# Optimization experiments

Measured on AMD Instinct MI355X. Metric: run time of the kernel, lower is better.

Reference implementation:

```python
import jax, jax.numpy as jnp
import numpy as np

N_NODES = 50000
N_EDGES = 800000
IN_SIZE = 128
HIDDEN = 128   # out_size * 2
OUT_SIZE = 64


def setup_inputs() -> dict:
    key = jax.random.key(0)
    ks = jax.random.split(key, 6)
    h = jax.random.normal(ks[0], (N_NODES, IN_SIZE), dtype=jnp.float32)
    W1 = jax.random.normal(ks[1], (IN_SIZE, HIDDEN), dtype=jnp.float32) * (1.0 / np.sqrt(IN_SIZE))
    b1 = jnp.zeros((HIDDEN,), dtype=jnp.float32)
    W2 = jax.random.normal(ks[2], (HIDDEN, OUT_SIZE), dtype=jnp.float32) * (1.0 / np.sqrt(HIDDEN))
    b2 = jnp.zeros((OUT_SIZE,), dtype=jnp.float32)
    src = jax.random.randint(ks[3], (N_EDGES,), 0, N_NODES, dtype=jnp.int64)
    dst = jax.random.randint(ks[4], (N_EDGES,), 0, N_NODES, dtype=jnp.int64)
    return {"h": h, "W1": W1, "b1": b1, "W2": W2, "b2": b2, "src": src, "dst": dst}


def _norms(src, dst, n_nodes):
    # DGL GraphConv norm='both': scale by out_degree^{-1/2} (src side)
    # and in_degree^{-1/2} (dst side); zero degrees clamped to 1.
    ones = jnp.ones(src.shape, dtype=jnp.float32)
    out_deg = jnp.maximum(jax.ops.segment_sum(ones, src, num_segments=n_nodes), 1.0)
    in_deg = jnp.maximum(jax.ops.segment_sum(ones, dst, num_segments=n_nodes), 1.0)
    return (out_deg ** -0.5)[:, None], (in_deg ** -0.5)[:, None]


def _graph_conv(x, W, b, src, dst, norm_out, norm_in, n_nodes):
    # h' = D_in^{-1/2} A D_out^{-1/2} x W + b
    x = x * norm_out                                   # [N, F]
    agg = jax.ops.segment_sum(x[src], dst, num_segments=n_nodes)  # SpMM: [N, F]
    return (agg * norm_in) @ W + b


def reference(h, W1, b1, W2, b2, src, dst):
    n_nodes = h.shape[0]
    norm_out, norm_in = _norms(src, dst, n_nodes)
    h = jax.nn.relu(_graph_conv(h, W1, b1, src, dst, norm_out, norm_in, n_nodes))
    h = jax.nn.relu(_graph_conv(h, W2, b2, src, dst, norm_out, norm_in, n_nodes))
    return h
```

## Files before the change

### kernel.cpp

```cpp
#include <hip/hip_runtime.h>

#define N_NODES 50000
#define N_EDGES 800000
#define CHUNKS 128
#define CHUNK_EDGES 6250
#define NBS 196
#define GA_BLOCKS 391
#define PLACE_BLOCKS 3125

typedef __attribute__((ext_vector_type(8))) short bf16x8;
typedef __attribute__((ext_vector_type(4))) float f32x4;

static __device__ inline unsigned short bf16_rne(float x) {
    unsigned ua = __float_as_uint(x);
    return (unsigned short)((ua + 0x7fffu + ((ua >> 16) & 1u)) >> 16);
}

static __device__ inline unsigned short f16_bits(float x) {
    _Float16 hx = (_Float16)x;
    return __builtin_bit_cast(unsigned short, hx);
}

static __device__ inline float2 unpack_f16x2(unsigned u) {
    _Float16 lo = __builtin_bit_cast(_Float16, (unsigned short)(u & 0xffffu));
    _Float16 hi = __builtin_bit_cast(_Float16, (unsigned short)(u >> 16));
    return make_float2((float)lo, (float)hi);
}

__global__ __launch_bounds__(1024) void hist_wpack_kernel(const int* __restrict__ src,
                                                          const int* __restrict__ dst,
                                                          unsigned char* __restrict__ cntD,
                                                          unsigned char* __restrict__ cntS,
                                                          unsigned char* __restrict__ rp,
                                                          const float* __restrict__ W1,
                                                          const float* __restrict__ W2,
                                                          unsigned short* __restrict__ wf_hi,
                                                          unsigned short* __restrict__ wf_lo,
                                                          unsigned short* __restrict__ wf2_hi,
                                                          unsigned short* __restrict__ wf2_lo) {
    const int t = threadIdx.x;
    const int c = blockIdx.x;

    if (c >= CHUNKS) {
        int idx = (c - CHUNKS) * 1024 + t;
        if (idx < 2048) {
            int l  = idx & 63;
            int ct = (idx >> 6) & 7;
            int ks = idx >> 9;
            int col = ct * 16 + (l & 15);
            int k0  = ks * 32 + (l >> 4) * 8;
            unsigned short hi[8], lo[8];
            #pragma unroll
            for (int j = 0; j < 8; ++j) {
                float x = W1[(size_t)(k0 + j) * 128 + col];
                unsigned short h16 = bf16_rne(x);
                hi[j] = h16;
                lo[j] = bf16_rne(x - __uint_as_float((unsigned)h16 << 16));
            }
            ((uint4*)wf_hi)[idx] = *(const uint4*)hi;
            ((uint4*)wf_lo)[idx] = *(const uint4*)lo;
        } else if (idx < 3072) {
            int i2 = idx - 2048;
            int l  = i2 & 63;
            int ct = (i2 >> 6) & 3;
            int ks = i2 >> 8;
            int col = ct * 16 + (l & 15);
            int k0  = ks * 32 + (l >> 4) * 8;
            unsigned short hi[8], lo[8];
            #pragma unroll
            for (int j = 0; j < 8; ++j) {
                float x = W2[(size_t)(k0 + j) * 64 + col];
                unsigned short h16 = bf16_rne(x);
                hi[j] = h16;
                lo[j] = bf16_rne(x - __uint_as_float((unsigned)h16 << 16));
            }
            ((uint4*)wf2_hi)[i2] = *(const uint4*)hi;
            ((uint4*)wf2_lo)[i2] = *(const uint4*)lo;
        }
        return;
    }

    __shared__ unsigned hD[12500];
    __shared__ unsigned hS[12500];
    for (int i = t; i < 12500; i += 1024) { hD[i] = 0u; hS[i] = 0u; }
    __syncthreads();

    const int base = c * CHUNK_EDGES;
    for (int i = t; i < CHUNK_EDGES; i += 1024) {
        int e = base + i;
        int d = dst[e];
        int s = src[e];
        unsigned shd = (unsigned)(d & 3) * 8u;
        unsigned old = atomicAdd(&hD[d >> 2], 1u << shd);
        rp[e] = (unsigned char)((old >> shd) & 0xffu);
        atomicAdd(&hS[s >> 2], 1u << ((unsigned)(s & 3) * 8u));
    }
    __syncthreads();

    unsigned* gD = (unsigned*)cntD + (size_t)c * 12500;
    unsigned* gS = (unsigned*)cntS + (size_t)c * 12500;
    for (int i = t; i < 12500; i += 1024) { gD[i] = hD[i]; gS[i] = hS[i]; }
}

__global__ __launch_bounds__(256) void deg_scan_kernel(unsigned char* __restrict__ cntD,
                                                       const unsigned char* __restrict__ cntS,
                                                       int* __restrict__ row_ptr,
                                                       int* __restrict__ bsum,
                                                       float* __restrict__ norm_out,
                                                       float* __restrict__ norm_in) {
    const int t = threadIdx.x, lane = t & 63, w = t >> 6;
    const int n = blockIdx.x * 256 + t;
    unsigned sumD = 0u, sumS = 0u;
    if (n < N_NODES) {
        #pragma unroll 4
        for (int c = 0; c < CHUNKS; ++c) {
            size_t idx = (size_t)c * 50000 + n;
            unsigned v = cntD[idx];
            cntD[idx] = (unsigned char)sumD;
            sumD += v;
            sumS += cntS[idx];
        }
        norm_in[n]  = rsqrtf((float)(sumD ? sumD : 1u));
        norm_out[n] = rsqrtf((float)(sumS ? sumS : 1u));
    }
    __shared__ int wsum[4];
    int v = (n < N_NODES) ? (int)sumD : 0;
    int incl = v;
    #pragma unroll
    for (int d = 1; d < 64; d <<= 1) {
        int u = __shfl_up(incl, d, 64);
        if (lane >= d) incl += u;
    }
    if (lane == 63) wsum[w] = incl;
    __syncthreads();
    int woff = 0, total = 0;
    #pragma unroll
    for (int j = 0; j < 4; ++j) {
        int s = wsum[j];
        if (j < w) woff += s;
        total += s;
    }
    if (n < N_NODES) row_ptr[n] = woff + incl - v;
    if (t == 0) bsum[blockIdx.x] = total;
}

__global__ __launch_bounds__(64) void scan2_kernel(int* __restrict__ bsum,
                                                   int* __restrict__ row_ptr) {
    const int lane = threadIdx.x;
    int carry = 0;
    for (int base = 0; base < NBS; base += 64) {
        int t = base + lane;
        int v = (t < NBS) ? bsum[t] : 0;
        int incl = v;
        #pragma unroll
        for (int d = 1; d < 64; d <<= 1) {
            int u = __shfl_up(incl, d, 64);
            if (lane >= d) incl += u;
        }
        int excl = carry + incl - v;
        if (t < NBS) bsum[t] = excl;
        if (t == NBS - 1) row_ptr[N_NODES] = N_EDGES - excl;
        carry += __shfl(incl, 63, 64);
    }
}

__global__ __launch_bounds__(256) void gemmA_place_kernel(const float* __restrict__ h,
                                                          const unsigned short* __restrict__ wf_hi,
                                                          const unsigned short* __restrict__ wf_lo,
                                                          const float* __restrict__ norm_out,
                                                          unsigned short* __restrict__ t1,
                                                          const int* __restrict__ src,
                                                          const int* __restrict__ dst,
                                                          const int* __restrict__ row_ptr,
                                                          const int* __restrict__ bsum,
                                                          const unsigned char* __restrict__ cntD,
                                                          const unsigned char* __restrict__ rp,
                                                          int* __restrict__ eidx) {
    if (blockIdx.x >= GA_BLOCKS) {
        int e = (blockIdx.x - GA_BLOCKS) * 256 + threadIdx.x;
        if (e < N_EDGES) {
            int d = dst[e];
            int c = e / CHUNK_EDGES;
            int pos = row_ptr[d] + bsum[d >> 8] + (int)cntD[(size_t)c * 50000 + d]
                    + (int)rp[e];
            eidx[pos] = src[e];
        }
        return;
    }

    const int t  = threadIdx.x;
    const int wv = t >> 6;
    const int l  = t & 63;
    const int lrow = l & 15;
    const int g    = l >> 4;
    const int n0 = blockIdx.x * 128 + wv * 32;

    int r0 = n0 + lrow;      if (r0 > N_NODES - 1) r0 = N_NODES - 1;
    int r1 = n0 + 16 + lrow; if (r1 > N_NODES - 1) r1 = N_NODES - 1;
    const float* h0 = h + (size_t)r0 * 128 + g * 8;
    const float* h1 = h + (size_t)r1 * 128 + g * 8;

    f32x4 acc[2][8];
    #pragma unroll
    for (int rt = 0; rt < 2; ++rt)
        #pragma unroll
        for (int ct = 0; ct < 8; ++ct)
            acc[rt][ct] = (f32x4){0.f, 0.f, 0.f, 0.f};

    const bf16x8* bh_base = (const bf16x8*)wf_hi;
    const bf16x8* bl_base = (const bf16x8*)wf_lo;

    for (int ks = 0; ks < 4; ++ks) {
        float a0[8], a1[8];
        *(float4*)(a0)     = *(const float4*)(h0 + ks * 32);
        *(float4*)(a0 + 4) = *(const float4*)(h0 + ks * 32 + 4);
        *(float4*)(a1)     = *(const float4*)(h1 + ks * 32);
        *(float4*)(a1 + 4) = *(const float4*)(h1 + ks * 32 + 4);

        bf16x8 a0h, a0l, a1h, a1l;
        #pragma unroll
        for (int j = 0; j < 8; ++j) {
            unsigned short hh = bf16_rne(a0[j]);
            a0h[j] = (short)hh;
            a0l[j] = (short)bf16_rne(a0[j] - __uint_as_float((unsigned)hh << 16));
            unsigned short h2 = bf16_rne(a1[j]);
            a1h[j] = (short)h2;
            a1l[j] = (short)bf16_rne(a1[j] - __uint_as_float((unsigned)h2 << 16));
        }

        #pragma unroll
        for (int ct = 0; ct < 8; ++ct) {
            const int fi = (ks * 8 + ct) * 64 + l;
            bf16x8 bh = bh_base[fi];
            bf16x8 bl = bl_base[fi];
            acc[0][ct] = __builtin_amdgcn_mfma_f32_16x16x32_bf16(a0l, bh, acc[0][ct], 0, 0, 0);
            acc[0][ct] = __builtin_amdgcn_mfma_f32_16x16x32_bf16(a0h, bl, acc[0][ct], 0, 0, 0);
            acc[0][ct] = __builtin_amdgcn_mfma_f32_16x16x32_bf16(a0h, bh, acc[0][ct], 0, 0, 0);
            acc[1][ct] = __builtin_amdgcn_mfma_f32_16x16x32_bf16(a1l, bh, acc[1][ct], 0, 0, 0);
            acc[1][ct] = __builtin_amdgcn_mfma_f32_16x16x32_bf16(a1h, bl, acc[1][ct], 0, 0, 0);
            acc[1][ct] = __builtin_amdgcn_mfma_f32_16x16x32_bf16(a1h, bh, acc[1][ct], 0, 0, 0);
        }
    }

    #pragma unroll
    for (int rt = 0; rt < 2; ++rt) {
        float no_[4];
        #pragma unroll
        for (int r = 0; r < 4; ++r) {
            int row = n0 + rt * 16 + g * 4 + r;
            no_[r] = (row < N_NODES) ? norm_out[row] : 0.f;
        }
        #pragma unroll
        for (int ct = 0; ct < 8; ++ct) {
            #pragma unroll
            for (int r = 0; r < 4; ++r) {
                int row = n0 + rt * 16 + g * 4 + r;
                if (row < N_NODES)
                    t1[(size_t)row * 128 + ct * 16 + lrow] = bf16_rne(acc[rt][ct][r] * no_[r]);
            }
        }
    }
}

__global__ __launch_bounds__(256) void gemmB_kernel(const float* __restrict__ h1p,
                                                    const unsigned short* __restrict__ wf2_hi,
                                                    const unsigned short* __restrict__ wf2_lo,
                                                    unsigned short* __restrict__ t2h) {
    const int t  = threadIdx.x;
    const int wv = t >> 6;
    const int l  = t & 63;
    const int lrow = l & 15;
    const int g    = l >> 4;
    const int n0 = blockIdx.x * 128 + wv * 32;

    int r0 = n0 + lrow;      if (r0 > N_NODES - 1) r0 = N_NODES - 1;
    int r1 = n0 + 16 + lrow; if (r1 > N_NODES - 1) r1 = N_NODES - 1;
    const float* h0 = h1p + (size_t)r0 * 128 + g * 8;
    const float* h1 = h1p + (size_t)r1 * 128 + g * 8;

    f32x4 acc[2][4];
    #pragma unroll
    for (int rt = 0; rt < 2; ++rt)
        #pragma unroll
        for (int ct = 0; ct < 4; ++ct)
            acc[rt][ct] = (f32x4){0.f, 0.f, 0.f, 0.f};

    const bf16x8* bh_base = (const bf16x8*)wf2_hi;
    const bf16x8* bl_base = (const bf16x8*)wf2_lo;

    for (int ks = 0; ks < 4; ++ks) {
        float a0[8], a1[8];
        *(float4*)(a0)     = *(const float4*)(h0 + ks * 32);
        *(float4*)(a0 + 4) = *(const float4*)(h0 + ks * 32 + 4);
        *(float4*)(a1)     = *(const float4*)(h1 + ks * 32);
        *(float4*)(a1 + 4) = *(const float4*)(h1 + ks * 32 + 4);

        bf16x8 a0h, a0l, a1h, a1l;
        #pragma unroll
        for (int j = 0; j < 8; ++j) {
            unsigned short hh = bf16_rne(a0[j]);
            a0h[j] = (short)hh;
            a0l[j] = (short)bf16_rne(a0[j] - __uint_as_float((unsigned)hh << 16));
            unsigned short h2 = bf16_rne(a1[j]);
            a1h[j] = (short)h2;
            a1l[j] = (short)bf16_rne(a1[j] - __uint_as_float((unsigned)h2 << 16));
        }

        #pragma unroll
        for (int ct = 0; ct < 4; ++ct) {
            const int fi = (ks * 4 + ct) * 64 + l;
            bf16x8 bh = bh_base[fi];
            bf16x8 bl = bl_base[fi];
            acc[0][ct] = __builtin_amdgcn_mfma_f32_16x16x32_bf16(a0l, bh, acc[0][ct], 0, 0, 0);
            acc[0][ct] = __builtin_amdgcn_mfma_f32_16x16x32_bf16(a0h, bl, acc[0][ct], 0, 0, 0);
            acc[0][ct] = __builtin_amdgcn_mfma_f32_16x16x32_bf16(a0h, bh, acc[0][ct], 0, 0, 0);
            acc[1][ct] = __builtin_amdgcn_mfma_f32_16x16x32_bf16(a1l, bh, acc[1][ct], 0, 0, 0);
            acc[1][ct] = __builtin_amdgcn_mfma_f32_16x16x32_bf16(a1h, bl, acc[1][ct], 0, 0, 0);
            acc[1][ct] = __builtin_amdgcn_mfma_f32_16x16x32_bf16(a1h, bh, acc[1][ct], 0, 0, 0);
        }
    }

    #pragma unroll
    for (int rt = 0; rt < 2; ++rt) {
        #pragma unroll
        for (int ct = 0; ct < 4; ++ct) {
            #pragma unroll
            for (int r = 0; r < 4; ++r) {
                int row = n0 + rt * 16 + g * 4 + r;
                if (row < N_NODES)
                    t2h[(size_t)row * 64 + ct * 16 + lrow] = f16_bits(acc[rt][ct][r]);
            }
        }
    }
}

__global__ __launch_bounds__(256) void pull128_kernel(const unsigned short* __restrict__ xb,
                                                      const int* __restrict__ row_ptr,
                                                      const int* __restrict__ bsum,
                                                      const int* __restrict__ eidx,
                                                      const float* __restrict__ b1,
                                                      const float* __restrict__ norm_in,
                                                      const float* __restrict__ norm_out,
                                                      float* __restrict__ out) {
    int node = blockIdx.x * 4 + (threadIdx.x >> 6);
    node = __builtin_amdgcn_readfirstlane(node);
    const int lane = threadIdx.x & 63;
    const int beg = __builtin_amdgcn_readfirstlane(row_ptr[node] + bsum[node >> 8]);
    const int end = __builtin_amdgcn_readfirstlane(row_ptr[node + 1] + bsum[(node + 1) >> 8]);

    float2 acc0 = make_float2(0.f, 0.f);
    float2 acc1 = make_float2(0.f, 0.f);
    float2 acc2 = make_float2(0.f, 0.f);
    float2 acc3 = make_float2(0.f, 0.f);

    for (int base = beg; base < end; base += 64) {
        const int cnt = min(64, end - base);
        int my_e = (lane < cnt) ? eidx[base + lane] : 0;
        int k = 0;
        for (; k + 7 < cnt; k += 8) {
            int s0 = __builtin_amdgcn_readlane(my_e, k);
            int s1 = __builtin_amdgcn_readlane(my_e, k + 1);
            int s2 = __builtin_amdgcn_readlane(my_e, k + 2);
            int s3 = __builtin_amdgcn_readlane(my_e, k + 3);
            int s4 = __builtin_amdgcn_readlane(my_e, k + 4);
            int s5 = __builtin_amdgcn_readlane(my_e, k + 5);
            int s6 = __builtin_amdgcn_readlane(my_e, k + 6);
            int s7 = __builtin_amdgcn_readlane(my_e, k + 7);
            unsigned u0 = ((const unsigned*)(xb + (size_t)s0 * 128))[lane];
            unsigned u1 = ((const unsigned*)(xb + (size_t)s1 * 128))[lane];
            unsigned u2 = ((const unsigned*)(xb + (size_t)s2 * 128))[lane];
            unsigned u3 = ((const unsigned*)(xb + (size_t)s3 * 128))[lane];
            unsigned u4 = ((const unsigned*)(xb + (size_t)s4 * 128))[lane];
            unsigned u5 = ((const unsigned*)(xb + (size_t)s5 * 128))[lane];
            unsigned u6 = ((const unsigned*)(xb + (size_t)s6 * 128))[lane];
            unsigned u7 = ((const unsigned*)(xb + (size_t)s7 * 128))[lane];
            acc0.x += __uint_as_float(u0 << 16);
            acc0.y += __uint_as_float(u0 & 0xffff0000u);
            acc1.x += __uint_as_float(u1 << 16);
            acc1.y += __uint_as_float(u1 & 0xffff0000u);
            acc2.x += __uint_as_float(u2 << 16);
            acc2.y += __uint_as_float(u2 & 0xffff0000u);
            acc3.x += __uint_as_float(u3 << 16);
            acc3.y += __uint_as_float(u3 & 0xffff0000u);
            acc0.x += __uint_as_float(u4 << 16);
            acc0.y += __uint_as_float(u4 & 0xffff0000u);
            acc1.x += __uint_as_float(u5 << 16);
            acc1.y += __uint_as_float(u5 & 0xffff0000u);
            acc2.x += __uint_as_float(u6 << 16);
            acc2.y += __uint_as_float(u6 & 0xffff0000u);
            acc3.x += __uint_as_float(u7 << 16);
            acc3.y += __uint_as_float(u7 & 0xffff0000u);
        }
        for (; k + 3 < cnt; k += 4) {
            int s0 = __builtin_amdgcn_readlane(my_e, k);
            int s1 = __builtin_amdgcn_readlane(my_e, k + 1);
            int s2 = __builtin_amdgcn_readlane(my_e, k + 2);
            int s3 = __builtin_amdgcn_readlane(my_e, k + 3);
            unsigned u0 = ((const unsigned*)(xb + (size_t)s0 * 128))[lane];
            unsigned u1 = ((const unsigned*)(xb + (size_t)s1 * 128))[lane];
            unsigned u2 = ((const unsigned*)(xb + (size_t)s2 * 128))[lane];
            unsigned u3 = ((const unsigned*)(xb + (size_t)s3 * 128))[lane];
            acc0.x += __uint_as_float(u0 << 16);
            acc0.y += __uint_as_float(u0 & 0xffff0000u);
            acc1.x += __uint_as_float(u1 << 16);
            acc1.y += __uint_as_float(u1 & 0xffff0000u);
            acc2.x += __uint_as_float(u2 << 16);
            acc2.y += __uint_as_float(u2 & 0xffff0000u);
            acc3.x += __uint_as_float(u3 << 16);
            acc3.y += __uint_as_float(u3 & 0xffff0000u);
        }
        for (; k < cnt; ++k) {
            int s0 = __builtin_amdgcn_readlane(my_e, k);
            unsigned u0 = ((const unsigned*)(xb + (size_t)s0 * 128))[lane];
            acc0.x += __uint_as_float(u0 << 16);
            acc0.y += __uint_as_float(u0 & 0xffff0000u);
        }
    }

    float ni = norm_in[node];
    float no = norm_out[node];
    float2 bb = ((const float2*)b1)[lane];
    float sx = (acc0.x + acc1.x) + (acc2.x + acc3.x);
    float sy = (acc0.y + acc1.y) + (acc2.y + acc3.y);
    float2 r;
    r.x = fmaxf(fmaf(sx, ni, bb.x), 0.f) * no;
    r.y = fmaxf(fmaf(sy, ni, bb.y), 0.f) * no;
    ((float2*)(out + (size_t)node * 128))[lane] = r;
}

__global__ __launch_bounds__(256) void pull64_kernel(const unsigned* __restrict__ x,
                                                     const int* __restrict__ row_ptr,
                                                     const int* __restrict__ bsum,
                                                     const int* __restrict__ eidx,
                                                     const float* __restrict__ b2,
                                                     const float* __restrict__ norm_in,
                                                     float* __restrict__ out) {
    int node = blockIdx.x * 4 + (threadIdx.x >> 6);
    node = __builtin_amdgcn_readfirstlane(node);
    const int lane = threadIdx.x & 63;
    const int half = lane >> 5;
    const int fl = lane & 31;
    const int beg = __builtin_amdgcn_readfirstlane(row_ptr[node] + bsum[node >> 8]);
    const int end = __builtin_amdgcn_readfirstlane(row_ptr[node + 1] + bsum[(node + 1) >> 8]);

    float2 a0 = make_float2(0.f, 0.f);
    float2 a1 = make_float2(0.f, 0.f);
    float2 a2 = make_float2(0.f, 0.f);
    float2 a3 = make_float2(0.f, 0.f);

    for (int base = beg; base < end; base += 64) {
        const int cnt = min(64, end - base);
        int my_e = (lane < cnt) ? eidx[base + lane] : 0;
        int k = 0;
        for (; k + 7 < cnt; k += 8) {
            int sa0 = __builtin_amdgcn_readlane(my_e, k);
            int sb0 = __builtin_amdgcn_readlane(my_e, k + 1);
            int sa1 = __builtin_amdgcn_readlane(my_e, k + 2);
            int sb1 = __builtin_amdgcn_readlane(my_e, k + 3);
            int sa2 = __builtin_amdgcn_readlane(my_e, k + 4);
            int sb2 = __builtin_amdgcn_readlane(my_e, k + 5);
            int sa3 = __builtin_amdgcn_readlane(my_e, k + 6);
            int sb3 = __builtin_amdgcn_readlane(my_e, k + 7);
            int e0 = half ? sb0 : sa0;
            int e1 = half ? sb1 : sa1;
            int e2 = half ? sb2 : sa2;
            int e3 = half ? sb3 : sa3;
            unsigned u0 = x[(size_t)e0 * 32 + fl];
            unsigned u1 = x[(size_t)e1 * 32 + fl];
            unsigned u2 = x[(size_t)e2 * 32 + fl];
            unsigned u3 = x[(size_t)e3 * 32 + fl];
            float2 v0 = unpack_f16x2(u0);
            float2 v1 = unpack_f16x2(u1);
            float2 v2 = unpack_f16x2(u2);
            float2 v3 = unpack_f16x2(u3);
            a0.x += v0.x; a0.y += v0.y;
            a1.x += v1.x; a1.y += v1.y;
            a2.x += v2.x; a2.y += v2.y;
            a3.x += v3.x; a3.y += v3.y;
        }
        for (; k + 1 < cnt; k += 2) {
            int sa = __builtin_amdgcn_readlane(my_e, k);
            int sb = __builtin_amdgcn_readlane(my_e, k + 1);
            int e0 = half ? sb : sa;
            unsigned u = x[(size_t)e0 * 32 + fl];
            float2 v = unpack_f16x2(u);
            a0.x += v.x; a0.y += v.y;
        }
        if (k < cnt) {
            int sa = __builtin_amdgcn_readlane(my_e, k);
            if (half == 0) {
                unsigned u = x[(size_t)sa * 32 + fl];
                float2 v = unpack_f16x2(u);
                a0.x += v.x; a0.y += v.y;
            }
        }
    }

    float ax = (a0.x + a1.x) + (a2.x + a3.x);
    float ay = (a0.y + a1.y) + (a2.y + a3.y);
    ax += __shfl_xor(ax, 32, 64);
    ay += __shfl_xor(ay, 32, 64);
    if (half == 0) {
        float ni = norm_in[node];
        float2 bb = ((const float2*)b2)[fl];
        float2 r;
        r.x = fmaxf(fmaf(ax, ni, bb.x), 0.f);
        r.y = fmaxf(fmaf(ay, ni, bb.y), 0.f);
        ((float2*)(out + (size_t)node * 64))[fl] = r;
    }
}

extern "C" void kernel_launch(void* const* d_in, const int* in_sizes, int n_in,
                              void* d_out, int out_size, void* d_ws, size_t ws_size,
                              hipStream_t stream) {
    const float* h  = (const float*)d_in[0];
    const float* W1 = (const float*)d_in[1];
    const float* b1 = (const float*)d_in[2];
    const float* W2 = (const float*)d_in[3];
    const float* b2 = (const float*)d_in[4];
    const int* src  = (const int*)d_in[5];
    const int* dst  = (const int*)d_in[6];
    float* out = (float*)d_out;

    char* ws = (char*)d_ws;
    size_t off = 0;
    auto alloc = [&](size_t bytes) {
        void* p = ws + off;
        off = (off + bytes + 255) & ~(size_t)255;
        return p;
    };
    float* norm_out   = (float*)alloc(N_NODES * sizeof(float));
    float* norm_in    = (float*)alloc(N_NODES * sizeof(float));
    int* row_ptr      = (int*)alloc((N_NODES + 1) * sizeof(int));
    int* bsum         = (int*)alloc(NBS * sizeof(int));
    unsigned short* wf_hi  = (unsigned short*)alloc(2048 * 16);
    unsigned short* wf_lo  = (unsigned short*)alloc(2048 * 16);
    unsigned short* wf2_hi = (unsigned short*)alloc(1024 * 16);
    unsigned short* wf2_lo = (unsigned short*)alloc(1024 * 16);
    int* eidx         = (int*)alloc((size_t)N_EDGES * sizeof(int));
    unsigned short* t1 = (unsigned short*)alloc((size_t)N_NODES * 128 * sizeof(short));
    float* h1p        = (float*)alloc((size_t)N_NODES * 128 * sizeof(float));

    unsigned char* cntD = (unsigned char*)h1p;
    unsigned char* cntS = cntD + (size_t)CHUNKS * 50000;
    unsigned char* rp   = cntS + (size_t)CHUNKS * 50000;
    unsigned short* t2h = t1;

    hist_wpack_kernel<<<CHUNKS + 3, 1024, 0, stream>>>(src, dst, cntD, cntS, rp,
                                                       W1, W2, wf_hi, wf_lo, wf2_hi, wf2_lo);

    deg_scan_kernel<<<NBS, 256, 0, stream>>>(cntD, cntS, row_ptr, bsum, norm_out, norm_in);

    scan2_kernel<<<1, 64, 0, stream>>>(bsum, row_ptr);

    gemmA_place_kernel<<<GA_BLOCKS + PLACE_BLOCKS, 256, 0, stream>>>(
        h, wf_hi, wf_lo, norm_out, t1, src, dst, row_ptr, bsum, cntD, rp, eidx);

    pull128_kernel<<<N_NODES / 4, 256, 0, stream>>>(t1, row_ptr, bsum, eidx, b1,
                                                    norm_in, norm_out, h1p);

    gemmB_kernel<<<GA_BLOCKS, 256, 0, stream>>>(h1p, wf2_hi, wf2_lo, t2h);

    pull64_kernel<<<N_NODES / 4, 256, 0, stream>>>((const unsigned*)t2h, row_ptr, bsum, eidx,
                                                   b2, norm_in, out);
}
```

Baseline: 203.6 us.

## Store layer-1 activations in fp16 and split histogram blocks by node half

The layer-1 output written by pull128 and read by gemmB is now stored as packed fp16 instead of fp32, halving that intermediate's write and read traffic. The histogram kernel is split into two blocks per edge chunk, each covering half the node range. That halves the shared-memory footprint per block, which should allow more resident blocks, at the cost of each block reading the edges twice and filtering them. Storing fp16 adds rounding error to the intermediate activations before the hi/lo bf16 split in gemmB.

```diff
diff --git a/kernel.cpp b/kernel.cpp
--- a/kernel.cpp
+++ b/kernel.cpp
@@ -19,6 +19,10 @@
 static __device__ inline unsigned short f16_bits(float x) {
     _Float16 hx = (_Float16)x;
     return __builtin_bit_cast(unsigned short, hx);
+}
+
+static __device__ inline float f16_val(unsigned short u) {
+    return (float)__builtin_bit_cast(_Float16, u);
 }
 
 static __device__ inline float2 unpack_f16x2(unsigned u) {
@@ -39,10 +43,10 @@
                                                           unsigned short* __restrict__ wf2_hi,
                                                           unsigned short* __restrict__ wf2_lo) {
     const int t = threadIdx.x;
-    const int c = blockIdx.x;
-
-    if (c >= CHUNKS) {
-        int idx = (c - CHUNKS) * 1024 + t;
+    const int b = blockIdx.x;
+
+    if (b >= 2 * CHUNKS) {
+        int idx = (b - 2 * CHUNKS) * 1024 + t;
         if (idx < 2048) {
             int l  = idx & 63;
             int ct = (idx >> 6) & 7;
@@ -80,9 +84,13 @@
         return;
     }
 
-    __shared__ unsigned hD[12500];
-    __shared__ unsigned hS[12500];
-    for (int i = t; i < 12500; i += 1024) { hD[i] = 0u; hS[i] = 0u; }
+    const int c    = b >> 1;
+    const int half = b & 1;
+    const int nbase = half * 25000;
+
+    __shared__ unsigned hD[6250];
+    __shared__ unsigned hS[6250];
+    for (int i = t; i < 6250; i += 1024) { hD[i] = 0u; hS[i] = 0u; }
     __syncthreads();
 
     const int base = c * CHUNK_EDGES;
@@ -90,16 +98,21 @@
         int e = base + i;
         int d = dst[e];
         int s = src[e];
-        unsigned shd = (unsigned)(d & 3) * 8u;
-        unsigned old = atomicAdd(&hD[d >> 2], 1u << shd);
-        rp[e] = (unsigned char)((old >> shd) & 0xffu);
-        atomicAdd(&hS[s >> 2], 1u << ((unsigned)(s & 3) * 8u));
+        unsigned dn = (unsigned)(d - nbase);
+        if (dn < 25000u) {
+            unsigned shd = (dn & 3u) * 8u;
+            unsigned old = atomicAdd(&hD[dn >> 2], 1u << shd);
+            rp[e] = (unsigned char)((old >> shd) & 0xffu);
+        }
+        unsigned sn = (unsigned)(s - nbase);
+        if (sn < 25000u)
+            atomicAdd(&hS[sn >> 2], 1u << ((sn & 3u) * 8u));
     }
     __syncthreads();
 
-    unsigned* gD = (unsigned*)cntD + (size_t)c * 12500;
-    unsigned* gS = (unsigned*)cntS + (size_t)c * 12500;
-    for (int i = t; i < 12500; i += 1024) { gD[i] = hD[i]; gS[i] = hS[i]; }
+    unsigned* gD = (unsigned*)cntD + (size_t)c * 12500 + half * 6250;
+    unsigned* gS = (unsigned*)cntS + (size_t)c * 12500 + half * 6250;
+    for (int i = t; i < 6250; i += 1024) { gD[i] = hD[i]; gS[i] = hS[i]; }
 }
 
 __global__ __launch_bounds__(256) void deg_scan_kernel(unsigned char* __restrict__ cntD,
@@ -262,7 +275,7 @@
     }
 }
 
-__global__ __launch_bounds__(256) void gemmB_kernel(const float* __restrict__ h1p,
+__global__ __launch_bounds__(256) void gemmB_kernel(const unsigned short* __restrict__ h1p16,
                                                     const unsigned short* __restrict__ wf2_hi,
                                                     const unsigned short* __restrict__ wf2_lo,
                                                     unsigned short* __restrict__ t2h) {
@@ -275,8 +288,8 @@
 
     int r0 = n0 + lrow;      if (r0 > N_NODES - 1) r0 = N_NODES - 1;
     int r1 = n0 + 16 + lrow; if (r1 > N_NODES - 1) r1 = N_NODES - 1;
-    const float* h0 = h1p + (size_t)r0 * 128 + g * 8;
-    const float* h1 = h1p + (size_t)r1 * 128 + g * 8;
+    const unsigned short* h0 = h1p16 + (size_t)r0 * 128 + g * 8;
+    const unsigned short* h1 = h1p16 + (size_t)r1 * 128 + g * 8;
 
     f32x4 acc[2][4];
     #pragma unroll
@@ -289,21 +302,21 @@
     const bf16x8* bl_base = (const bf16x8*)wf2_lo;
 
     for (int ks = 0; ks < 4; ++ks) {
-        float a0[8], a1[8];
-        *(float4*)(a0)     = *(const float4*)(h0 + ks * 32);
-        *(float4*)(a0 + 4) = *(const float4*)(h0 + ks * 32 + 4);
-        *(float4*)(a1)     = *(const float4*)(h1 + ks * 32);
-        *(float4*)(a1 + 4) = *(const float4*)(h1 + ks * 32 + 4);
+        unsigned short a0u[8], a1u[8];
+        *(uint4*)a0u = *(const uint4*)(h0 + ks * 32);
+        *(uint4*)a1u = *(const uint4*)(h1 + ks * 32);
 
         bf16x8 a0h, a0l, a1h, a1l;
         #pragma unroll
         for (int j = 0; j < 8; ++j) {
-            unsigned short hh = bf16_rne(a0[j]);
+            float x0 = f16_val(a0u[j]);
+            unsigned short hh = bf16_rne(x0);
             a0h[j] = (short)hh;
-            a0l[j] = (short)bf16_rne(a0[j] - __uint_as_float((unsigned)hh << 16));
-            unsigned short h2 = bf16_rne(a1[j]);
+            a0l[j] = (short)bf16_rne(x0 - __uint_as_float((unsigned)hh << 16));
+            float x1 = f16_val(a1u[j]);
+            unsigned short h2 = bf16_rne(x1);
             a1h[j] = (short)h2;
-            a1l[j] = (short)bf16_rne(a1[j] - __uint_as_float((unsigned)h2 << 16));
+            a1l[j] = (short)bf16_rne(x1 - __uint_as_float((unsigned)h2 << 16));
         }
 
         #pragma unroll
@@ -341,7 +354,7 @@
                                                       const float* __restrict__ b1,
                                                       const float* __restrict__ norm_in,
                                                       const float* __restrict__ norm_out,
-                                                      float* __restrict__ out) {
+                                                      unsigned* __restrict__ out16) {
     int node = blockIdx.x * 4 + (threadIdx.x >> 6);
     node = __builtin_amdgcn_readfirstlane(node);
     const int lane = threadIdx.x & 63;
@@ -422,10 +435,10 @@
     float2 bb = ((const float2*)b1)[lane];
     float sx = (acc0.x + acc1.x) + (acc2.x + acc3.x);
     float sy = (acc0.y + acc1.y) + (acc2.y + acc3.y);
-    float2 r;
-    r.x = fmaxf(fmaf(sx, ni, bb.x), 0.f) * no;
-    r.y = fmaxf(fmaf(sy, ni, bb.y), 0.f) * no;
-    ((float2*)(out + (size_t)node * 128))[lane] = r;
+    float rx = fmaxf(fmaf(sx, ni, bb.x), 0.f) * no;
+    float ry = fmaxf(fmaf(sy, ni, bb.y), 0.f) * no;
+    unsigned pw = (unsigned)f16_bits(rx) | ((unsigned)f16_bits(ry) << 16);
+    out16[(size_t)node * 64 + lane] = pw;
 }
 
 __global__ __launch_bounds__(256) void pull64_kernel(const unsigned* __restrict__ x,
@@ -539,15 +552,17 @@
     unsigned short* wf2_lo = (unsigned short*)alloc(1024 * 16);
     int* eidx         = (int*)alloc((size_t)N_EDGES * sizeof(int));
     unsigned short* t1 = (unsigned short*)alloc((size_t)N_NODES * 128 * sizeof(short));
-    float* h1p        = (float*)alloc((size_t)N_NODES * 128 * sizeof(float));
-
-    unsigned char* cntD = (unsigned char*)h1p;
+    unsigned char* scratch = (unsigned char*)alloc(26 * 1024 * 1024);
+
+    unsigned char* cntD = scratch;
     unsigned char* cntS = cntD + (size_t)CHUNKS * 50000;
     unsigned char* rp   = cntS + (size_t)CHUNKS * 50000;
+    unsigned short* h1p16 = (unsigned short*)scratch;
     unsigned short* t2h = t1;
 
-    hist_wpack_kernel<<<CHUNKS + 3, 1024, 0, stream>>>(src, dst, cntD, cntS, rp,
-                                                       W1, W2, wf_hi, wf_lo, wf2_hi, wf2_lo);
+    hist_wpack_kernel<<<2 * CHUNKS + 3, 1024, 0, stream>>>(src, dst, cntD, cntS, rp,
+                                                           W1, W2, wf_hi, wf_lo,
+                                                           wf2_hi, wf2_lo);
 
     deg_scan_kernel<<<NBS, 256, 0, stream>>>(cntD, cntS, row_ptr, bsum, norm_out, norm_in);
 
@@ -557,9 +572,9 @@
         h, wf_hi, wf_lo, norm_out, t1, src, dst, row_ptr, bsum, cntD, rp, eidx);
 
     pull128_kernel<<<N_NODES / 4, 256, 0, stream>>>(t1, row_ptr, bsum, eidx, b1,
-                                                    norm_in, norm_out, h1p);
-
-    gemmB_kernel<<<GA_BLOCKS, 256, 0, stream>>>(h1p, wf2_hi, wf2_lo, t2h);
+                                                    norm_in, norm_out, (unsigned*)h1p16);
+
+    gemmB_kernel<<<GA_BLOCKS, 256, 0, stream>>>(h1p16, wf2_hi, wf2_lo, t2h);
 
     pull64_kernel<<<N_NODES / 4, 256, 0, stream>>>((const unsigned*)t2h, row_ptr, bsum, eidx,
                                                    b2, norm_in, out);
```

New measurement: 201.7 us (median of 2 runs). No clear change (-1.0%).
